# Kernel optimization log

Measured on AMD Instinct MI355X. Metric: run time of the kernel, lower is better.

Reference implementation:

```python
import jax, jax.numpy as jnp
import numpy as np

E = 768      # embed_dim (hidden_size)
H = 12       # num_attention_heads
DH = E // H  # head_dim = 64
B, S = 8, 1024


def setup_inputs() -> dict:
    key = jax.random.key(0)
    ks = jax.random.split(key, 10)
    sc = 1.0 / np.sqrt(E)
    inp = {
        "hidden_state": jax.random.normal(ks[0], (B, S, E), dtype=jnp.float32),
        # per-head Q/K/V projections, stacked over heads: [H, E, DH]
        "Wq": jax.random.normal(ks[1], (H, E, DH), dtype=jnp.float32) * sc,
        "bq": jax.random.normal(ks[2], (H, DH), dtype=jnp.float32) * 0.02,
        "Wk": jax.random.normal(ks[3], (H, E, DH), dtype=jnp.float32) * sc,
        "bk": jax.random.normal(ks[4], (H, DH), dtype=jnp.float32) * 0.02,
        "Wv": jax.random.normal(ks[5], (H, E, DH), dtype=jnp.float32) * sc,
        "bv": jax.random.normal(ks[6], (H, DH), dtype=jnp.float32) * 0.02,
        # output projection: [E, E]
        "Wo": jax.random.normal(ks[7], (E, E), dtype=jnp.float32) * sc,
        "bo": jax.random.normal(ks[8], (E,), dtype=jnp.float32) * 0.02,
    }
    return inp


def reference(hidden_state, Wq, bq, Wk, bk, Wv, bv, Wo, bo):
    # Q/K/V per head: [B,S,E] x [H,E,D] -> [B,H,S,D]
    q = jnp.einsum("bse,hed->bhsd", hidden_state, Wq) + bq[None, :, None, :]
    k = jnp.einsum("bse,hed->bhsd", hidden_state, Wk) + bk[None, :, None, :]
    v = jnp.einsum("bse,hed->bhsd", hidden_state, Wv) + bv[None, :, None, :]
    scale = 1.0 / jnp.sqrt(jnp.asarray(DH, dtype=q.dtype))
    scores = jnp.einsum("bhsd,bhtd->bhst", q, k) * scale   # [B,H,S,S]
    weights = jax.nn.softmax(scores, axis=-1)
    attn = jnp.einsum("bhst,bhtd->bhsd", weights, v)        # [B,H,S,D]
    # concat heads (head order matches ModuleList concat): [B,S,H*D]=[B,S,E]
    x = attn.transpose(0, 2, 1, 3).reshape(hidden_state.shape[0], hidden_state.shape[1], E)
    return x @ Wo + bo
```

## Files before the change

### kernel.cpp

```cpp
#include <hip/hip_runtime.h>

typedef unsigned short u16;
typedef __bf16 bf16;
typedef bf16 bf16x8 __attribute__((ext_vector_type(8)));
typedef float f32x4 __attribute__((ext_vector_type(4)));
typedef u16 u16x4 __attribute__((ext_vector_type(4)));
typedef u16 u16x8 __attribute__((ext_vector_type(8)));

#define MROWS 8192
#define EDIM 768
#define NQKV 2304
#define NHEAD 12
#define DH 64
#define SEQ 1024
#define BATCH 8
#define BH 96
#define BHSD (BH * SEQ * DH)
#define KIT64 (EDIM / 64)

#if __has_builtin(__builtin_amdgcn_exp2f)
#define EXP2(x) __builtin_amdgcn_exp2f(x)
#else
#define EXP2(x) exp2f(x)
#endif

__device__ __forceinline__ u16 f2bf(float f) {
  bf16 b = (bf16)f;
  return __builtin_bit_cast(u16, b);
}

__device__ __forceinline__ void gload_lds16(const u16* g, u16* l) {
  __builtin_amdgcn_global_load_lds(
      (const __attribute__((address_space(1))) void*)g,
      (__attribute__((address_space(3))) void*)l, 16, 0, 0);
}

__global__ __launch_bounds__(256) void prep(
    const float* __restrict__ x, u16* __restrict__ xb,
    const float* __restrict__ Wq, const float* __restrict__ Wk,
    const float* __restrict__ Wv, const float* __restrict__ Wo,
    u16* __restrict__ Wt, u16* __restrict__ Wot) {
  int bid = blockIdx.x;
  int tid = threadIdx.x;
  if (bid >= 576) {
    int i = ((bid - 576) * 256 + tid) * 4;
    float4 v = *(const float4*)(x + i);
    u16x4 o;
    o[0] = f2bf(v.x); o[1] = f2bf(v.y); o[2] = f2bf(v.z); o[3] = f2bf(v.w);
    *(u16x4*)(xb + i) = o;
    return;
  }
  __shared__ float T[64][65];
  int c = tid & 63, r4 = tid >> 6;
  if (bid < 432) {
    int region = bid / 144, rem = bid - region * 144;
    int h = rem / 12, e0 = (rem - h * 12) * 64;
    const float* W = region == 0 ? Wq : (region == 1 ? Wk : Wv);
    for (int p = 0; p < 16; p++) {
      int er = r4 + p * 4;
      T[er][c] = W[(size_t)(h * EDIM + e0 + er) * DH + c];
    }
    __syncthreads();
    int nbase = region * EDIM + h * 64;
    for (int p = 0; p < 16; p++) {
      int dr = r4 + p * 4;
      Wt[(size_t)(nbase + dr) * EDIM + e0 + c] = f2bf(T[c][dr]);
    }
  } else {
    int bo2 = bid - 432;
    int n0 = (bo2 / 12) * 64, e0 = (bo2 - (bo2 / 12) * 12) * 64;
    for (int p = 0; p < 16; p++) {
      int er = r4 + p * 4;
      T[er][c] = Wo[(size_t)(e0 + er) * EDIM + n0 + c];
    }
    __syncthreads();
    for (int p = 0; p < 16; p++) {
      int dr = r4 + p * 4;
      Wot[(size_t)(n0 + dr) * EDIM + e0 + c] = f2bf(T[c][dr]);
    }
  }
}

template <int BM, int BN, int NW>
__device__ __forceinline__ void gemm_core(
    const u16* __restrict__ A, const u16* __restrict__ Bt,
    u16* As, u16* Bs, int m0, int n0, int tid, f32x4 acc[4][4]) {
  constexpr int NT = NW * 64;
  constexpr int RPP = NT / 8;
  constexpr int AP = BM / RPP;
  constexpr int BP = BN / RPP;
  constexpr int WMN = BM / 64;
  int wv = __builtin_amdgcn_readfirstlane(tid >> 6);
  int lane = tid & 63, quad = lane >> 4, l16 = lane & 15;
  int wm = (wv % WMN) * 64, wn = (wv / WMN) * 64;
  int srow = tid >> 3, cpos = tid & 7;
  int swcol = (cpos ^ (srow & 7)) * 8;
  const u16* Ag = A + (size_t)(m0 + srow) * EDIM + swcol;
  const u16* Bg = Bt + (size_t)(n0 + srow) * EDIM + swcol;
  u16* Asl = As + srow * 64 + cpos * 8;
  u16* Bsl = Bs + srow * 64 + cpos * 8;

  for (int k = 0; k < KIT64; k++) {
    __syncthreads();
    const u16* ak = Ag + k * 64;
    const u16* bk = Bg + k * 64;
#pragma unroll
    for (int p = 0; p < AP; p++)
      gload_lds16(ak + (size_t)(p * RPP) * EDIM, Asl + p * RPP * 64);
#pragma unroll
    for (int p = 0; p < BP; p++)
      gload_lds16(bk + (size_t)(p * RPP) * EDIM, Bsl + p * RPP * 64);
    __syncthreads();
#pragma unroll
    for (int kh = 0; kh < 2; kh++) {
      bf16x8 af[4], bfr[4];
      for (int i = 0; i < 4; i++) {
        int row = wm + i * 16 + l16;
        af[i] = *(const bf16x8*)(As + row * 64 + (((kh * 4 + quad) ^ (row & 7))) * 8);
      }
      for (int j = 0; j < 4; j++) {
        int row = wn + j * 16 + l16;
        bfr[j] = *(const bf16x8*)(Bs + row * 64 + (((kh * 4 + quad) ^ (row & 7))) * 8);
      }
      for (int i = 0; i < 4; i++)
        for (int j = 0; j < 4; j++)
          acc[i][j] = __builtin_amdgcn_mfma_f32_16x16x32_bf16(af[i], bfr[j], acc[i][j], 0, 0, 0);
    }
  }
}

__global__ __launch_bounds__(256, 4) void gemm_qkv(
    const u16* __restrict__ A, const u16* __restrict__ Bt,
    const float* __restrict__ bq, const float* __restrict__ bk, const float* __restrict__ bv,
    u16* __restrict__ qkv) {
  __shared__ __align__(16) u16 As[128 * 64];
  __shared__ __align__(16) u16 Bs[128 * 64];
  int tid = threadIdx.x;
  int wv = tid >> 6, lane = tid & 63, quad = lane >> 4, l16 = lane & 15;
  int wm = (wv & 1) * 64, wn = (wv >> 1) * 64;
  int lin = blockIdx.y * 64 + blockIdx.x;
  int xcd = lin & 7, r8 = lin >> 3;
  int m0 = (xcd * 8 + (r8 & 7)) * 128;
  int n0 = (r8 >> 3) * 128;
  f32x4 acc[4][4] = {};
  gemm_core<128, 128, 4>(A, Bt, As, Bs, m0, n0, tid, acc);

  const float kQscale = 0.18033688011112042f;
  for (int i = 0; i < 4; i++) {
    int row0 = m0 + wm + i * 16 + quad * 4;
    for (int j = 0; j < 4; j++) {
      int n = n0 + wn + j * 16 + l16;
      int region = n / EDIM;
      int hd = n - region * EDIM;
      int h = hd >> 6, d = hd & 63;
      const float* bp = region == 0 ? bq : (region == 1 ? bk : bv);
      float bias = bp[hd];
      float scale = region == 0 ? kQscale : 1.0f;
      for (int r4 = 0; r4 < 4; r4++) {
        int rr = row0 + r4;
        int bb = rr >> 10, s = rr & 1023;
        float val = (acc[i][j][r4] + bias) * scale;
        u16 bv16 = f2bf(val);
        int bhh = bb * NHEAD + h;
        if (region < 2) {
          qkv[(size_t)region * BHSD + ((size_t)bhh * SEQ + s) * DH + d] = bv16;
        } else {
          qkv[(size_t)2 * BHSD + ((size_t)bhh * DH + d) * SEQ + s] = bv16;
        }
      }
    }
  }
}

__global__ __launch_bounds__(256, 3) void attn_kernel(const u16* __restrict__ qkv, u16* __restrict__ attn) {
  int lin = blockIdx.y * 96 + blockIdx.x;
  int xcd = lin & 7, rr = lin >> 3;
  int bh = xcd * 12 + (rr >> 3);
  int qt = rr & 7;
  int b = bh / NHEAD, h = bh - b * NHEAD;
  const u16* Q  = qkv + (size_t)bh * SEQ * DH;
  const u16* K  = qkv + (size_t)(BH + bh) * SEQ * DH;
  const u16* VT = qkv + (size_t)(2 * BH + bh) * SEQ * DH;
  int tid = threadIdx.x, wave = tid >> 6, lane = tid & 63, quad = lane >> 4, l16 = lane & 15;
  int q_base = qt * 128 + wave * 32;

  __shared__ __align__(16) u16 Ks[2][64 * 64];
  __shared__ __align__(16) u16 Vts[2][64 * 64];
  __shared__ __align__(16) u16 Ps[4][32 * 64];

  bf16x8 qf[2][2];
  for (int g = 0; g < 2; g++)
    for (int c = 0; c < 2; c++)
      qf[g][c] = *(const bf16x8*)(Q + (size_t)(q_base + g * 16 + l16) * DH + c * 32 + quad * 8);

  f32x4 o[2][4] = {};
  float psum[2][4] = {};

  int tr = tid >> 3, cpos = tid & 7;
  int ssw = (cpos ^ (tr & 7)) * 8;
  const u16* Kg0 = K + (size_t)tr * DH + ssw;
  const u16* Kg1 = K + (size_t)(tr + 32) * DH + ssw;
  const u16* Vg0 = VT + (size_t)tr * SEQ + ssw;
  const u16* Vg1 = VT + (size_t)(tr + 32) * SEQ + ssw;
  int dst0 = tr * 64 + cpos * 8;
  int dst1 = (tr + 32) * 64 + cpos * 8;

  gload_lds16(Kg0, Ks[0] + dst0);
  gload_lds16(Kg1, Ks[0] + dst1);
  gload_lds16(Vg0, Vts[0] + dst0);
  gload_lds16(Vg1, Vts[0] + dst1);
  __syncthreads();

  int buf = 0;
  u16* P = Ps[wave];
  for (int t0 = 0; t0 < SEQ; t0 += 64) {
    if (t0 + 64 < SEQ) {
      int nb = buf ^ 1;
      gload_lds16(Kg0 + (size_t)(t0 + 64) * DH, Ks[nb] + dst0);
      gload_lds16(Kg1 + (size_t)(t0 + 64) * DH, Ks[nb] + dst1);
      gload_lds16(Vg0 + t0 + 64, Vts[nb] + dst0);
      gload_lds16(Vg1 + t0 + 64, Vts[nb] + dst1);
    }
    const u16* Kb = Ks[buf];
    const u16* Vb = Vts[buf];

    __builtin_amdgcn_s_setprio(1);
    for (int tc = 0; tc < 4; tc++) {
      int krow = tc * 16 + l16, k7 = l16 & 7;
      bf16x8 kf0 = *(const bf16x8*)(Kb + krow * 64 + ((quad ^ k7) * 8));
      bf16x8 kf1 = *(const bf16x8*)(Kb + krow * 64 + (((4 + quad) ^ k7) * 8));
      int pc = tc * 2 + (l16 >> 3);
      for (int g = 0; g < 2; g++) {
        f32x4 z = {};
        z = __builtin_amdgcn_mfma_f32_16x16x32_bf16(qf[g][0], kf0, z, 0, 0, 0);
        z = __builtin_amdgcn_mfma_f32_16x16x32_bf16(qf[g][1], kf1, z, 0, 0, 0);
        for (int r = 0; r < 4; r++) {
          float pv = EXP2(z[r]);
          psum[g][r] += pv;
          int prow = g * 16 + quad * 4 + r;
          P[prow * 64 + ((pc ^ (prow & 7)) * 8) + (l16 & 7)] = f2bf(pv);
        }
      }
    }
    __builtin_amdgcn_s_setprio(0);

    bf16x8 pf[2][2];
    for (int g = 0; g < 2; g++)
      for (int kc = 0; kc < 2; kc++)
        pf[g][kc] = *(const bf16x8*)(P + (g * 16 + l16) * 64 + (((kc * 4 + quad) ^ (l16 & 7)) * 8));

    __builtin_amdgcn_s_setprio(1);
    for (int n = 0; n < 4; n++) {
      int vrow = n * 16 + l16, v7 = l16 & 7;
      bf16x8 vf0 = *(const bf16x8*)(Vb + vrow * 64 + ((quad ^ v7) * 8));
      bf16x8 vf1 = *(const bf16x8*)(Vb + vrow * 64 + (((4 + quad) ^ v7) * 8));
      for (int g = 0; g < 2; g++) {
        o[g][n] = __builtin_amdgcn_mfma_f32_16x16x32_bf16(pf[g][0], vf0, o[g][n], 0, 0, 0);
        o[g][n] = __builtin_amdgcn_mfma_f32_16x16x32_bf16(pf[g][1], vf1, o[g][n], 0, 0, 0);
      }
    }
    __builtin_amdgcn_s_setprio(0);

    __syncthreads();
    buf ^= 1;
  }

  for (int g = 0; g < 2; g++) {
    for (int m = 1; m < 16; m <<= 1)
      for (int r = 0; r < 4; r++)
        psum[g][r] += __shfl_xor(psum[g][r], m);
    for (int r = 0; r < 4; r++) {
      float inv = 1.0f / psum[g][r];
      int qrow = q_base + g * 16 + quad * 4 + r;
      size_t rowoff = (size_t)(b * SEQ + qrow) * EDIM + h * DH;
      for (int n = 0; n < 4; n++)
        attn[rowoff + n * 16 + l16] = f2bf(o[g][n][r] * inv);
    }
  }
}

__global__ __launch_bounds__(128, 3) void gemm_out(
    const u16* __restrict__ A, const u16* __restrict__ Bt,
    const float* __restrict__ bo, float* __restrict__ out) {
  __shared__ __align__(16) u16 As[64 * 64];
  __shared__ __align__(16) u16 Bs[128 * 64];
  int tid = threadIdx.x;
  int wv = tid >> 6, lane = tid & 63, quad = lane >> 4, l16 = lane & 15;
  int wn = wv * 64;
  int lin = blockIdx.y * 128 + blockIdx.x;
  int xcd = lin & 7, r = lin >> 3;
  int m0 = (xcd * 16 + (r & 15)) * 64;
  int n0 = (r >> 4) * 128;
  f32x4 acc[4][4] = {};
  gemm_core<64, 128, 2>(A, Bt, As, Bs, m0, n0, tid, acc);

  for (int i = 0; i < 4; i++) {
    int row0 = m0 + i * 16 + quad * 4;
    for (int j = 0; j < 4; j++) {
      int n = n0 + wn + j * 16 + l16;
      float bias = bo[n];
      for (int r4 = 0; r4 < 4; r4++)
        out[(size_t)(row0 + r4) * EDIM + n] = acc[i][j][r4] + bias;
    }
  }
}

extern "C" void kernel_launch(void* const* d_in, const int* in_sizes, int n_in,
                              void* d_out, int out_size, void* d_ws, size_t ws_size,
                              hipStream_t stream) {
  const float* x  = (const float*)d_in[0];
  const float* Wq = (const float*)d_in[1];
  const float* bq = (const float*)d_in[2];
  const float* Wk = (const float*)d_in[3];
  const float* bk = (const float*)d_in[4];
  const float* Wv = (const float*)d_in[5];
  const float* bv = (const float*)d_in[6];
  const float* Wo = (const float*)d_in[7];
  const float* bo = (const float*)d_in[8];
  float* out = (float*)d_out;
  char* ws = (char*)d_ws;

  u16* Xb   = (u16*)(ws);
  u16* Wt   = (u16*)(ws + 12582912);
  u16* Wot  = (u16*)(ws + 16121856);
  u16* qkv  = (u16*)(ws + 17301504);
  u16* attn = (u16*)(ws + 55050240);

  prep<<<6720, 256, 0, stream>>>(x, Xb, Wq, Wk, Wv, Wo, Wt, Wot);
  gemm_qkv<<<dim3(64, 18), 256, 0, stream>>>(Xb, Wt, bq, bk, bv, qkv);
  attn_kernel<<<dim3(96, 8), 256, 0, stream>>>(qkv, attn);
  gemm_out<<<dim3(128, 6), 128, 0, stream>>>(attn, Wot, bo, out);
}
```

Baseline: 195.5 us.

## Load K and V fragments directly from global memory instead of LDS staging

The attention kernel drops the double-buffered LDS staging of K and V tiles along with the block-wide barrier per iteration. Each wave now reads its MFMA operand fragments for K and V^T straight from global memory into registers, relying on L2/L1 caching for reuse across the four waves and the other query-tile blocks. This removes LDS traffic and synchronization, but each wave issues redundant global loads. There is also no explicit prefetch, so load latency may be exposed.

```diff
diff --git a/kernel.cpp b/kernel.cpp
--- a/kernel.cpp
+++ b/kernel.cpp
@@ -184,8 +184,6 @@
   int tid = threadIdx.x, wave = tid >> 6, lane = tid & 63, quad = lane >> 4, l16 = lane & 15;
   int q_base = qt * 128 + wave * 32;
 
-  __shared__ __align__(16) u16 Ks[2][64 * 64];
-  __shared__ __align__(16) u16 Vts[2][64 * 64];
   __shared__ __align__(16) u16 Ps[4][32 * 64];
 
   bf16x8 qf[2][2];
@@ -196,39 +194,24 @@
   f32x4 o[2][4] = {};
   float psum[2][4] = {};
 
-  int tr = tid >> 3, cpos = tid & 7;
-  int ssw = (cpos ^ (tr & 7)) * 8;
-  const u16* Kg0 = K + (size_t)tr * DH + ssw;
-  const u16* Kg1 = K + (size_t)(tr + 32) * DH + ssw;
-  const u16* Vg0 = VT + (size_t)tr * SEQ + ssw;
-  const u16* Vg1 = VT + (size_t)(tr + 32) * SEQ + ssw;
-  int dst0 = tr * 64 + cpos * 8;
-  int dst1 = (tr + 32) * 64 + cpos * 8;
-
-  gload_lds16(Kg0, Ks[0] + dst0);
-  gload_lds16(Kg1, Ks[0] + dst1);
-  gload_lds16(Vg0, Vts[0] + dst0);
-  gload_lds16(Vg1, Vts[0] + dst1);
-  __syncthreads();
-
-  int buf = 0;
   u16* P = Ps[wave];
+  const u16* Kf = K + (size_t)l16 * DH + quad * 8;
+  const u16* Vf = VT + (size_t)l16 * SEQ + quad * 8;
+
   for (int t0 = 0; t0 < SEQ; t0 += 64) {
-    if (t0 + 64 < SEQ) {
-      int nb = buf ^ 1;
-      gload_lds16(Kg0 + (size_t)(t0 + 64) * DH, Ks[nb] + dst0);
-      gload_lds16(Kg1 + (size_t)(t0 + 64) * DH, Ks[nb] + dst1);
-      gload_lds16(Vg0 + t0 + 64, Vts[nb] + dst0);
-      gload_lds16(Vg1 + t0 + 64, Vts[nb] + dst1);
-    }
-    const u16* Kb = Ks[buf];
-    const u16* Vb = Vts[buf];
+    bf16x8 vf[4][2];
+#pragma unroll
+    for (int n = 0; n < 4; n++) {
+      vf[n][0] = *(const bf16x8*)(Vf + (size_t)(n * 16) * SEQ + t0);
+      vf[n][1] = *(const bf16x8*)(Vf + (size_t)(n * 16) * SEQ + t0 + 32);
+    }
 
     __builtin_amdgcn_s_setprio(1);
+#pragma unroll
     for (int tc = 0; tc < 4; tc++) {
-      int krow = tc * 16 + l16, k7 = l16 & 7;
-      bf16x8 kf0 = *(const bf16x8*)(Kb + krow * 64 + ((quad ^ k7) * 8));
-      bf16x8 kf1 = *(const bf16x8*)(Kb + krow * 64 + (((4 + quad) ^ k7) * 8));
+      const u16* kb = Kf + (size_t)(t0 + tc * 16) * DH;
+      bf16x8 kf0 = *(const bf16x8*)(kb);
+      bf16x8 kf1 = *(const bf16x8*)(kb + 32);
       int pc = tc * 2 + (l16 >> 3);
       for (int g = 0; g < 2; g++) {
         f32x4 z = {};
@@ -245,24 +228,19 @@
     __builtin_amdgcn_s_setprio(0);
 
     bf16x8 pf[2][2];
+#pragma unroll
     for (int g = 0; g < 2; g++)
       for (int kc = 0; kc < 2; kc++)
         pf[g][kc] = *(const bf16x8*)(P + (g * 16 + l16) * 64 + (((kc * 4 + quad) ^ (l16 & 7)) * 8));
 
     __builtin_amdgcn_s_setprio(1);
-    for (int n = 0; n < 4; n++) {
-      int vrow = n * 16 + l16, v7 = l16 & 7;
-      bf16x8 vf0 = *(const bf16x8*)(Vb + vrow * 64 + ((quad ^ v7) * 8));
-      bf16x8 vf1 = *(const bf16x8*)(Vb + vrow * 64 + (((4 + quad) ^ v7) * 8));
+#pragma unroll
+    for (int n = 0; n < 4; n++)
       for (int g = 0; g < 2; g++) {
-        o[g][n] = __builtin_amdgcn_mfma_f32_16x16x32_bf16(pf[g][0], vf0, o[g][n], 0, 0, 0);
-        o[g][n] = __builtin_amdgcn_mfma_f32_16x16x32_bf16(pf[g][1], vf1, o[g][n], 0, 0, 0);
-      }
-    }
+        o[g][n] = __builtin_amdgcn_mfma_f32_16x16x32_bf16(pf[g][0], vf[n][0], o[g][n], 0, 0, 0);
+        o[g][n] = __builtin_amdgcn_mfma_f32_16x16x32_bf16(pf[g][1], vf[n][1], o[g][n], 0, 0, 0);
+      }
     __builtin_amdgcn_s_setprio(0);
-
-    __syncthreads();
-    buf ^= 1;
   }
 
   for (int g = 0; g < 2; g++) {
```

Result: slower. 249.5 us (+27.6%).
